# Performance work log

Measured on AMD Instinct MI355X. Metric: run time of the kernel, lower is better.

Reference implementation:

```python
import jax, jax.numpy as jnp
import numpy as np


def setup_inputs() -> dict:
    key = jax.random.key(0)
    k1, k2 = jax.random.split(key)
    B, C, D = 16384, 4096, 1024
    feat = jax.random.normal(k1, (B, D), dtype=jnp.float32)
    centers = jax.random.normal(k2, (C, D), dtype=jnp.float32)
    return {"feat": feat, "centers": centers}


def reference(feat, centers):
    # Pairwise squared Euclidean distance: dist[b, c] = sum_d (feat[b,d] - centers[c,d])^2
    # materializing the O(B*C*D) broadcast difference (same math as the torch module).
    x2 = jnp.sum(feat * feat, axis=-1, keepdims=True)          # [B, 1]
    c2 = jnp.sum(centers * centers, axis=-1)[None, :]          # [1, C]
    xc = jnp.einsum("bd,cd->bc", feat, centers)                # [B, C] GEMM
    dist = x2 + c2 - 2.0 * xc
    return dist
```

## Files before the change

kernel.cpp:

```cpp
#include <hip/hip_runtime.h>
#include <hip/hip_bf16.h>

typedef __bf16 bf16x8 __attribute__((ext_vector_type(8)));
typedef float floatx4 __attribute__((ext_vector_type(4)));

__device__ __forceinline__ unsigned f2bf(float f) {
    unsigned u = __float_as_uint(f);
    u += 0x7FFFu + ((u >> 16) & 1u);
    return u >> 16;
}

__device__ __forceinline__ void gl2lds(const void* g, void* l) {
    void* gnc = const_cast<void*>(g);
    __builtin_amdgcn_global_load_lds(
        (__attribute__((address_space(1))) void*)gnc,
        (__attribute__((address_space(3))) void*)l,
        16, 0, 0);
}

__global__ __launch_bounds__(256) void cast_norm2(
    const float* __restrict__ feat, const float* __restrict__ cent,
    unsigned short* __restrict__ Ab, unsigned short* __restrict__ Bb,
    float* __restrict__ x2, float* __restrict__ c2, int M)
{
    const int wave = threadIdx.x >> 6;
    const int lane = threadIdx.x & 63;
    const int row  = blockIdx.x * 4 + wave;

    const float* src;
    unsigned short* dst;
    float* nrm;
    if (row < M) {
        src = feat + (size_t)row * 1024;
        dst = Ab   + (size_t)row * 1024;
        nrm = x2 + row;
    } else {
        const int r = row - M;
        src = cent + (size_t)r * 1024;
        dst = Bb   + (size_t)r * 1024;
        nrm = c2 + r;
    }

    const float4* s4 = (const float4*)src;
    uint2* d2 = (uint2*)dst;
    float s = 0.f;
#pragma unroll
    for (int j = 0; j < 4; ++j) {
        const float4 v = s4[j * 64 + lane];
        s += v.x * v.x + v.y * v.y + v.z * v.z + v.w * v.w;
        uint2 o;
        o.x = f2bf(v.x) | (f2bf(v.y) << 16);
        o.y = f2bf(v.z) | (f2bf(v.w) << 16);
        d2[j * 64 + lane] = o;
    }
#pragma unroll
    for (int off = 32; off > 0; off >>= 1) s += __shfl_down(s, off);
    if (lane == 0) *nrm = s;
}

__global__ __launch_bounds__(512, 2) void dist_gemm(
    const unsigned short* __restrict__ A,
    const unsigned short* __restrict__ B,
    const float* __restrict__ x2,
    const float* __restrict__ c2,
    float* __restrict__ out,
    int M, int N)
{
    __shared__ alignas(16) char lds_raw[131072];
    char* ldsb = lds_raw;
    const char* ldsc = lds_raw;

    const int tid  = threadIdx.x;
    const int wave = tid >> 6;
    const int lane = tid & 63;
    const int quad = lane >> 4;
    const int l16  = lane & 15;
    const int wm   = wave >> 2;
    const int wn   = wave & 3;

    const int gx  = gridDim.x;
    const int lin = blockIdx.y * gx + blockIdx.x;
    const int colsPerXcd = gx >> 3;
    const int xcd  = lin & 7;
    const int slot = lin >> 3;
    const int bx = xcd * colsPerXcd + (slot % colsPerXcd);
    const int by = slot / colsPerXcd;

    const int blockRow = by * 256;
    const int blockCol = bx * 256;

    const int cswz = (lane & 3) ^ ((lane >> 3) & 3);
    const unsigned short* pA = A + (size_t)(blockRow + wave * 16 + (lane >> 2)) * 1024 + cswz * 8;
    const unsigned short* pB = B + (size_t)(blockCol + wave * 16 + (lane >> 2)) * 1024 + cswz * 8;
    const int stOff = wave * 1024;

#define STAGE_A(buf, kt) do {                                                 \
        const unsigned short* _s0 = pA + (size_t)(kt) * 64;                   \
        const unsigned short* _s1 = _s0 + 131072;                             \
        char* _d0 = ldsb + (buf) * 65536 + stOff;                             \
        gl2lds(_s0,      _d0);                                                \
        gl2lds(_s0 + 32, _d0 + 16384);                                        \
        gl2lds(_s1,      _d0 + 8192);                                         \
        gl2lds(_s1 + 32, _d0 + 8192 + 16384);                                 \
    } while (0)
#define STAGE_B(buf, kt, h) do {                                              \
        const unsigned short* _s = pB + (size_t)(h) * 131072 + (kt) * 64;     \
        char* _d = ldsb + (buf) * 65536 + 32768 + (h) * 8192 + stOff;         \
        gl2lds(_s,      _d);                                                  \
        gl2lds(_s + 32, _d + 16384);                                          \
    } while (0)

    const int swq = quad ^ ((l16 >> 1) & 3);
    const int aRd = (wm * 128 + l16) * 64 + swq * 16;
    const int bRd = 32768 + (wn * 64 + l16) * 64 + swq * 16;

#define RD_A(buf, ks, mf) (*(const bf16x8*)(ldsc + (buf) * 65536 + (ks) * 16384 + (mf) * 1024 + aRd))
#define RD_B(buf, ks, nf) (*(const bf16x8*)(ldsc + (buf) * 65536 + (ks) * 16384 + (nf) * 1024 + bRd))

#define LDA8(buf, mo) do {                                                    \
        aF[0] = RD_A(buf, 0, (mo) + 0); aF[2] = RD_A(buf, 0, (mo) + 1);       \
        aF[4] = RD_A(buf, 0, (mo) + 2); aF[6] = RD_A(buf, 0, (mo) + 3);       \
        aF[1] = RD_A(buf, 1, (mo) + 0); aF[3] = RD_A(buf, 1, (mo) + 1);       \
        aF[5] = RD_A(buf, 1, (mo) + 2); aF[7] = RD_A(buf, 1, (mo) + 3);       \
    } while (0)
#define LDB4(bb, buf, no) do {                                                \
        bb[0] = RD_B(buf, 0, (no) + 0); bb[2] = RD_B(buf, 0, (no) + 1);       \
        bb[1] = RD_B(buf, 1, (no) + 0); bb[3] = RD_B(buf, 1, (no) + 1);       \
    } while (0)

#define BAR()    do { __builtin_amdgcn_s_barrier(); asm volatile("" ::: "memory"); } while (0)
#define LGKM0()  asm volatile("s_waitcnt lgkmcnt(0)" ::: "memory")
#define VMCNT4() asm volatile("s_waitcnt vmcnt(4)" ::: "memory")
#define VMCNT0() asm volatile("s_waitcnt vmcnt(0)" ::: "memory")

#define MFMA_Q(mo, no, bb) do {                                               \
        __builtin_amdgcn_s_setprio(1);                                        \
        _Pragma("unroll")                                                     \
        for (int _m = 0; _m < 4; ++_m) {                                      \
            _Pragma("unroll")                                                 \
            for (int _n = 0; _n < 2; ++_n) {                                  \
                _Pragma("unroll")                                             \
                for (int _k = 0; _k < 2; ++_k) {                              \
                    acc[(mo) + _m][(no) + _n] =                               \
                        __builtin_amdgcn_mfma_f32_16x16x32_bf16(              \
                            aF[_m * 2 + _k], bb[_n * 2 + _k],                 \
                            acc[(mo) + _m][(no) + _n], 0, 0, 0);              \
                }                                                             \
            }                                                                 \
        }                                                                     \
        __builtin_amdgcn_s_setprio(0);                                        \
    } while (0)

    floatx4 acc[8][4];
#pragma unroll
    for (int i = 0; i < 8; ++i)
#pragma unroll
        for (int j = 0; j < 4; ++j) acc[i][j] = (floatx4){0.f, 0.f, 0.f, 0.f};

    bf16x8 aF[8], bL[4], bH[4];

#define HALF(buf, obuf, tB, tA, SB, SA, LASTVM) do {                          \
                                                                      \
        LDA8(buf, 0); LDB4(bL, buf, 0);                                       \
        if (SB) STAGE_B(obuf, tB, 0);                                         \
        LGKM0(); MFMA_Q(0, 0, bL); BAR();                                     \
                                                                      \
        LDB4(bH, buf, 2);                                                     \
        if (SB) STAGE_B(obuf, tB, 1);                                         \
        LGKM0(); MFMA_Q(0, 2, bH); BAR();                                     \
                                                                      \
        LDA8(buf, 4);                                                         \
        LGKM0(); MFMA_Q(4, 2, bH); BAR();                                     \
                                                                      \
        if (SA) STAGE_A(buf, tA);                                             \
        MFMA_Q(4, 0, bL);                                                     \
        if (SA) { VMCNT4(); } else { LASTVM; }                                \
        BAR();                                                                \
    } while (0)

    STAGE_A(0, 0);
    STAGE_B(0, 0, 0); STAGE_B(0, 0, 1);
    STAGE_A(1, 1);
    VMCNT4();
    BAR();

#pragma unroll 1
    for (int it = 0; it < 7; ++it) {
        const int T = it * 2;
        HALF(0, 1, T + 1, T + 2, true, true, (void)0);
        HALF(1, 0, T + 2, T + 3, true, true, (void)0);
    }
    HALF(0, 1, 15, 0, true, false, VMCNT0());
    HALF(1, 0, 0, 0, false, false, (void)0);

    float c2v[4];
#pragma unroll
    for (int nf = 0; nf < 4; ++nf) c2v[nf] = c2[blockCol + wn * 64 + nf * 16 + l16];

#pragma unroll
    for (int mf = 0; mf < 8; ++mf) {
        const int rowb = blockRow + wm * 128 + mf * 16 + quad * 4;
        float x2v[4];
#pragma unroll
        for (int r = 0; r < 4; ++r) x2v[r] = x2[rowb + r];
#pragma unroll
        for (int nf = 0; nf < 4; ++nf) {
            const int col = blockCol + wn * 64 + nf * 16 + l16;
            float* o = out + (size_t)rowb * N + col;
#pragma unroll
            for (int r = 0; r < 4; ++r)
                o[(size_t)r * N] = fmaf(-2.0f, acc[mf][nf][r], x2v[r] + c2v[nf]);
        }
    }

#undef HALF
#undef MFMA_Q
#undef VMCNT0
#undef VMCNT4
#undef LGKM0
#undef BAR
#undef LDB4
#undef LDA8
#undef RD_B
#undef RD_A
#undef STAGE_B
#undef STAGE_A
}

__global__ __launch_bounds__(256) void dist_fallback(
    const float* __restrict__ A, const float* __restrict__ B,
    float* __restrict__ out, int M, int N, int K)
{
    __shared__ float sA[64][17];
    __shared__ float sB[64][17];
    const int tid = threadIdx.x;
    const int tx = tid & 15;
    const int ty = tid >> 4;
    const int rowBase = blockIdx.y * 64;
    const int colBase = blockIdx.x * 64;
    float acc[4][4] = {};
    for (int k0 = 0; k0 < K; k0 += 16) {
        __syncthreads();
        {
            const int r = tid >> 2, c = (tid & 3) * 4;
            float4 va = *(const float4*)(A + (size_t)(rowBase + r) * K + k0 + c);
            sA[r][c] = va.x; sA[r][c + 1] = va.y; sA[r][c + 2] = va.z; sA[r][c + 3] = va.w;
            float4 vb = *(const float4*)(B + (size_t)(colBase + r) * K + k0 + c);
            sB[r][c] = vb.x; sB[r][c + 1] = vb.y; sB[r][c + 2] = vb.z; sB[r][c + 3] = vb.w;
        }
        __syncthreads();
#pragma unroll
        for (int kk = 0; kk < 16; kk++) {
            float ra[4], rb[4];
#pragma unroll
            for (int i = 0; i < 4; i++) ra[i] = sA[ty * 4 + i][kk];
#pragma unroll
            for (int j = 0; j < 4; j++) rb[j] = sB[tx * 4 + j][kk];
#pragma unroll
            for (int i = 0; i < 4; i++)
#pragma unroll
                for (int j = 0; j < 4; j++) {
                    float d = ra[i] - rb[j];
                    acc[i][j] = fmaf(d, d, acc[i][j]);
                }
        }
    }
#pragma unroll
    for (int i = 0; i < 4; i++)
#pragma unroll
        for (int j = 0; j < 4; j++)
            out[(size_t)(rowBase + ty * 4 + i) * N + (colBase + tx * 4 + j)] = acc[i][j];
}

extern "C" void kernel_launch(void* const* d_in, const int* in_sizes, int n_in,
                              void* d_out, int out_size, void* d_ws, size_t ws_size,
                              hipStream_t stream) {
    const float* feat = (const float*)d_in[0];
    const float* cent = (const float*)d_in[1];
    float* out = (float*)d_out;

    const int D = 1024;
    const int M = in_sizes[0] / D;
    const int N = in_sizes[1] / D;

    const size_t offA  = 0;
    const size_t offB  = offA + (size_t)M * D * sizeof(unsigned short);
    const size_t offX2 = offB + (size_t)N * D * sizeof(unsigned short);
    const size_t offC2 = offX2 + (size_t)M * sizeof(float);
    const size_t need  = offC2 + (size_t)N * sizeof(float);

    if (ws_size >= need && (M % 256) == 0 && (N % 2048) == 0) {
        unsigned short* Ab = (unsigned short*)((char*)d_ws + offA);
        unsigned short* Bb = (unsigned short*)((char*)d_ws + offB);
        float* x2 = (float*)((char*)d_ws + offX2);
        float* c2 = (float*)((char*)d_ws + offC2);

        cast_norm2<<<(M + N) / 4, 256, 0, stream>>>(feat, cent, Ab, Bb, x2, c2, M);
        dist_gemm<<<dim3(N / 256, M / 256), 512, 0, stream>>>(Ab, Bb, x2, c2, out, M, N);
    } else {
        dist_fallback<<<dim3(N / 64, M / 64), 256, 0, stream>>>(feat, cent, out, M, N, D);
    }
}
```

Baseline: 427.5 us.

## Stage GEMM tiles through registers with one barrier per K-tile

Replaces the direct global-to-LDS async loads with ordinary 16-byte global loads into registers. The registers are then written to the other LDS buffer with an XOR swizzle while MFMAs on the current buffer run. The four barriers and vmcnt waits per K-tile shrink to one lgkmcnt wait and one barrier, with a sched_barrier to keep the MFMA/ds_read ordering. This aims to cut synchronization stalls. In exchange it uses about 32 extra VGPRs for staging and adds explicit ds_write traffic.

```diff
diff --git a/kernel.cpp b/kernel.cpp
--- a/kernel.cpp
+++ b/kernel.cpp
@@ -8,14 +8,6 @@
     unsigned u = __float_as_uint(f);
     u += 0x7FFFu + ((u >> 16) & 1u);
     return u >> 16;
-}
-
-__device__ __forceinline__ void gl2lds(const void* g, void* l) {
-    void* gnc = const_cast<void*>(g);
-    __builtin_amdgcn_global_load_lds(
-        (__attribute__((address_space(1))) void*)gnc,
-        (__attribute__((address_space(3))) void*)l,
-        16, 0, 0);
 }
 
 __global__ __launch_bounds__(256) void cast_norm2(
@@ -89,25 +81,26 @@
     const int blockRow = by * 256;
     const int blockCol = bx * 256;
 
-    const int cswz = (lane & 3) ^ ((lane >> 3) & 3);
-    const unsigned short* pA = A + (size_t)(blockRow + wave * 16 + (lane >> 2)) * 1024 + cswz * 8;
-    const unsigned short* pB = B + (size_t)(blockCol + wave * 16 + (lane >> 2)) * 1024 + cswz * 8;
-    const int stOff = wave * 1024;
-
-#define STAGE_A(buf, kt) do {                                                 \
-        const unsigned short* _s0 = pA + (size_t)(kt) * 64;                   \
-        const unsigned short* _s1 = _s0 + 131072;                             \
-        char* _d0 = ldsb + (buf) * 65536 + stOff;                             \
-        gl2lds(_s0,      _d0);                                                \
-        gl2lds(_s0 + 32, _d0 + 16384);                                        \
-        gl2lds(_s1,      _d0 + 8192);                                         \
-        gl2lds(_s1 + 32, _d0 + 8192 + 16384);                                 \
-    } while (0)
-#define STAGE_B(buf, kt, h) do {                                              \
-        const unsigned short* _s = pB + (size_t)(h) * 131072 + (kt) * 64;     \
-        char* _d = ldsb + (buf) * 65536 + 32768 + (h) * 8192 + stOff;         \
-        gl2lds(_s,      _d);                                                  \
-        gl2lds(_s + 32, _d + 16384);                                          \
+    const int wks  = tid >> 8;
+    const int wrow = tid & 255;
+    const int rsw  = (wrow >> 1) & 3;
+    const int s0 = 0 ^ rsw, s1 = 1 ^ rsw, s2 = 2 ^ rsw, s3 = 3 ^ rsw;
+
+    const uint4* pAg = (const uint4*)(A + (size_t)(blockRow + wrow) * 1024 + wks * 32);
+    const uint4* pBg = (const uint4*)(B + (size_t)(blockCol + wrow) * 1024 + wks * 32);
+
+    uint4 vA[4], vB[4];
+
+#define LOADR() do {                                                          \
+        vA[0] = pAg[0]; vA[1] = pAg[1]; vA[2] = pAg[2]; vA[3] = pAg[3];       \
+        vB[0] = pBg[0]; vB[1] = pBg[1]; vB[2] = pBg[2]; vB[3] = pBg[3];       \
+        pAg += 8; pBg += 8;                                                   \
+    } while (0)
+#define DSW(nb) do {                                                          \
+        uint4* _wa = (uint4*)(ldsb + (nb) * 65536 + wks * 16384 + wrow * 64); \
+        uint4* _wb = (uint4*)(ldsb + (nb) * 65536 + 32768 + wks * 16384 + wrow * 64); \
+        _wa[s0] = vA[0]; _wa[s1] = vA[1]; _wa[s2] = vA[2]; _wa[s3] = vA[3];   \
+        _wb[s0] = vB[0]; _wb[s1] = vB[1]; _wb[s2] = vB[2]; _wb[s3] = vB[3];   \
     } while (0)
 
     const int swq = quad ^ ((l16 >> 1) & 3);
@@ -130,8 +123,6 @@
 
 #define BAR()    do { __builtin_amdgcn_s_barrier(); asm volatile("" ::: "memory"); } while (0)
 #define LGKM0()  asm volatile("s_waitcnt lgkmcnt(0)" ::: "memory")
-#define VMCNT4() asm volatile("s_waitcnt vmcnt(4)" ::: "memory")
-#define VMCNT0() asm volatile("s_waitcnt vmcnt(0)" ::: "memory")
 
 #define MFMA_Q(mo, no, bb) do {                                               \
         __builtin_amdgcn_s_setprio(1);                                        \
@@ -159,39 +150,30 @@
 
     bf16x8 aF[8], bL[4], bH[4];
 
-#define HALF(buf, obuf, tB, tA, SB, SA, LASTVM) do {                          \
-                                                                      \
-        LDA8(buf, 0); LDB4(bL, buf, 0);                                       \
-        if (SB) STAGE_B(obuf, tB, 0);                                         \
-        LGKM0(); MFMA_Q(0, 0, bL); BAR();                                     \
-                                                                      \
-        LDB4(bH, buf, 2);                                                     \
-        if (SB) STAGE_B(obuf, tB, 1);                                         \
-        LGKM0(); MFMA_Q(0, 2, bH); BAR();                                     \
-                                                                      \
-        LDA8(buf, 4);                                                         \
-        LGKM0(); MFMA_Q(4, 2, bH); BAR();                                     \
-                                                                      \
-        if (SA) STAGE_A(buf, tA);                                             \
+#define TILE(cur, DW, DL) do {                                                \
+        LDA8(cur, 0); LDB4(bL, cur, 0); LDB4(bH, cur, 2);                     \
+        MFMA_Q(0, 0, bL); MFMA_Q(0, 2, bH);                                   \
+        __builtin_amdgcn_sched_barrier(0);                                    \
+        LDA8(cur, 4);                                                         \
+        MFMA_Q(4, 2, bH);                                                     \
+        if (DW) DSW((cur) ^ 1);                                               \
+        if (DL) LOADR();                                                      \
         MFMA_Q(4, 0, bL);                                                     \
-        if (SA) { VMCNT4(); } else { LASTVM; }                                \
-        BAR();                                                                \
-    } while (0)
-
-    STAGE_A(0, 0);
-    STAGE_B(0, 0, 0); STAGE_B(0, 0, 1);
-    STAGE_A(1, 1);
-    VMCNT4();
-    BAR();
+        LGKM0(); BAR();                                                       \
+    } while (0)
+
+    LOADR();
+    DSW(0);
+    LOADR();
+    LGKM0(); BAR();
 
 #pragma unroll 1
     for (int it = 0; it < 7; ++it) {
-        const int T = it * 2;
-        HALF(0, 1, T + 1, T + 2, true, true, (void)0);
-        HALF(1, 0, T + 2, T + 3, true, true, (void)0);
-    }
-    HALF(0, 1, 15, 0, true, false, VMCNT0());
-    HALF(1, 0, 0, 0, false, false, (void)0);
+        TILE(0, true, true);
+        TILE(1, true, true);
+    }
+    TILE(0, true, false);
+    TILE(1, false, false);
 
     float c2v[4];
 #pragma unroll
@@ -213,18 +195,16 @@
         }
     }
 
-#undef HALF
+#undef TILE
 #undef MFMA_Q
-#undef VMCNT0
-#undef VMCNT4
 #undef LGKM0
 #undef BAR
 #undef LDB4
 #undef LDA8
 #undef RD_B
 #undef RD_A
-#undef STAGE_B
-#undef STAGE_A
+#undef DSW
+#undef LOADR
 }
 
 __global__ __launch_bounds__(256) void dist_fallback(
```

After: 650.2 us. 1.52x slower.
